# Kernel optimization log

Measured on AMD Instinct MI355X. Metric: run time of the kernel, lower is better.

Reference implementation:

```python
import jax, jax.numpy as jnp
import numpy as np

B, N, D, H, DEG = 2, 20000, 256, 8, 8
E = N * DEG
EPS = 1e-3  # keras LayerNormalization default epsilon


def layer_norm(x, gamma, beta):
    mu = jnp.mean(x, axis=-1, keepdims=True)
    var = jnp.mean(jnp.square(x - mu), axis=-1, keepdims=True)
    return (x - mu) * jax.lax.rsqrt(var + EPS) * gamma + beta


def setup_inputs() -> dict:
    key = jax.random.key(0)
    ks = jax.random.split(key, 8)
    x = jax.random.normal(ks[0], (B, N, D), dtype=jnp.float32)
    # edge list sorted by source node; every node has DEG out-edges so
    # segment_sum covers all N segments (matches tf.math.segment_sum semantics)
    src = jnp.repeat(jnp.arange(N, dtype=jnp.int64), DEG)
    dst = jax.random.randint(ks[1], (E,), 0, N, dtype=jnp.int64)
    edges = jnp.stack([src, dst], axis=1)  # [E, 2]
    scale = 0.05
    wq = jax.random.normal(ks[2], (D, D), dtype=jnp.float32) * scale
    wk = jax.random.normal(ks[3], (D, D), dtype=jnp.float32) * scale
    wv = jax.random.normal(ks[4], (D, D), dtype=jnp.float32) * scale
    wo = jax.random.normal(ks[5], (D, D), dtype=jnp.float32) * scale
    zeros = jnp.zeros((D,), dtype=jnp.float32)
    ones = jnp.ones((D,), dtype=jnp.float32)
    return {
        "x": x, "edges": edges,
        "wq": wq, "bq": zeros, "wk": wk, "bk": zeros,
        "wv": wv, "bv": zeros, "wo": wo, "bo": zeros,
        "gamma1": ones, "beta1": zeros, "gamma2": ones, "beta2": zeros,
    }


def reference(x, edges, wq, bq, wk, bk, wv, bv, wo, bo, gamma1, beta1, gamma2, beta2):
    b, n, d = x.shape
    h, dh = H, D // H
    xn = layer_norm(x, gamma1, beta1)                      # [B,N,D]
    # QKV projections, split heads, move node axis to front: [N,B,H,dh]
    def proj(w, bias):
        y = (xn @ w + bias).reshape(b, n, h, dh)
        return jnp.transpose(y, (1, 0, 2, 3))
    q, k, v = proj(wq, bq), proj(wk, bk), proj(wv, bv)
    src, dst = edges[:, 0], edges[:, 1]
    q_part = q[src]                                         # [E,B,H,dh]
    k_part = k[dst]
    v_part = v[dst]
    logits = jnp.sum(q_part * k_part, axis=-1, keepdims=True) / jnp.sqrt(
        jnp.asarray(dh, dtype=x.dtype))                     # [E,B,H,1]
    w = jnp.exp(logits)                                     # unnormalized softmax (as in source)
    num = jax.ops.segment_sum(v_part * w, src, num_segments=n)  # [N,B,H,dh]
    den = jax.ops.segment_sum(w, src, num_segments=n)           # [N,B,H,1]
    attn = num / den
    attn = jnp.transpose(attn, (1, 0, 2, 3)).reshape(b, n, d)   # [B,N,D]
    concat = xn + attn                                      # residual uses normed input (source reassigns `inputs`)
    out = layer_norm(concat, gamma2, beta2)
    out = jax.nn.relu(out @ wo + bo)
    return out + concat
```

## Files before the change

kernel.cpp:

```cpp
#include <hip/hip_runtime.h>
#include <hip/hip_bf16.h>

typedef __bf16 bf16x8 __attribute__((ext_vector_type(8)));
typedef float  f32x4  __attribute__((ext_vector_type(4)));

__device__ __forceinline__ float bf2f(unsigned short u) {
    union { unsigned int i; float f; } v; v.i = ((unsigned int)u) << 16; return v.f;
}
__device__ __forceinline__ unsigned short f2bf(float f) {
    union { float f; unsigned int i; } v; v.f = f;
    unsigned int x = v.i;
    unsigned int r = (x + 0x7FFFu + ((x >> 16) & 1u)) >> 16;
    return (unsigned short)r;
}

#define BF16_MAGIC 0x3F803F80u

template<bool BF16> __device__ __forceinline__ float ld1(const void* p, size_t i) {
    if constexpr (BF16) return bf2f(((const unsigned short*)p)[i]);
    else                return ((const float*)p)[i];
}
template<bool BF16> __device__ __forceinline__ float4 ld4v(const void* p, size_t i4) {
    if constexpr (BF16) {
        ushort4 u = ((const ushort4*)p)[i4];
        return make_float4(bf2f(u.x), bf2f(u.y), bf2f(u.z), bf2f(u.w));
    } else {
        return ((const float4*)p)[i4];
    }
}

#define NNODE 20000
#define ROWS  40000
#define DMODEL 256

template<bool BF16IN>
__global__ __launch_bounds__(256) void prep_kernel(
    const void* wq, const void* wk, const void* wv, const void* wo,
    const void* bq, const void* bk, const void* bv, const void* bo,
    const unsigned* __restrict__ mode,
    unsigned short* __restrict__ Wqkvt,
    unsigned short* __restrict__ Wot,
    float* __restrict__ biasq,
    float* __restrict__ biaso)
{
    if ((mode[0] == BF16_MAGIC) != BF16IN) return;
    int idx = blockIdx.x * 256 + threadIdx.x;
    if (idx < 768 * 256) {
        int n = idx >> 8, k = idx & 255;
        int sel = n >> 8, nl = n & 255;
        const void* w = (sel == 0) ? wq : (sel == 1) ? wk : wv;
        Wqkvt[idx] = f2bf(ld1<BF16IN>(w, k * 256 + nl));
    } else {
        int idx2 = idx - 768 * 256;
        int n = idx2 >> 8, k = idx2 & 255;
        Wot[idx2] = f2bf(ld1<BF16IN>(wo, k * 256 + n));
    }
    if (idx < 768) {
        const void* bb = (idx < 256) ? bq : (idx < 512) ? bk : bv;
        biasq[idx] = ld1<BF16IN>(bb, idx & 255);
    }
    if (idx >= 768 && idx < 1024) {
        biaso[idx - 768] = ld1<BF16IN>(bo, idx - 768);
    }
}

template<bool BF16IN>
__global__ __launch_bounds__(256) void ln1_kernel(
    const void* x, const void* g1, const void* b1,
    const unsigned* __restrict__ mode,
    unsigned short* __restrict__ xn)
{
    if ((mode[0] == BF16_MAGIC) != BF16IN) return;
    int wave = threadIdx.x >> 6, lane = threadIdx.x & 63;
    int m = blockIdx.x * 4 + wave;
    float4 f = ld4v<BF16IN>(x, (size_t)m * 64 + lane);
    float s  = f.x + f.y + f.z + f.w;
    float ss = f.x*f.x + f.y*f.y + f.z*f.z + f.w*f.w;
    #pragma unroll
    for (int mk = 1; mk < 64; mk <<= 1) { s += __shfl_xor(s, mk); ss += __shfl_xor(ss, mk); }
    float mu  = s * (1.f/256.f);
    float var = ss * (1.f/256.f) - mu*mu;
    float rs  = rsqrtf(var + 1e-3f);
    float4 g = ld4v<BF16IN>(g1, lane);
    float4 b = ld4v<BF16IN>(b1, lane);
    ushort4 o;
    o.x = f2bf((f.x - mu) * rs * g.x + b.x);
    o.y = f2bf((f.y - mu) * rs * g.y + b.y);
    o.z = f2bf((f.z - mu) * rs * g.z + b.z);
    o.w = f2bf((f.w - mu) * rs * g.w + b.w);
    *(ushort4*)(xn + (size_t)m * DMODEL + lane * 4) = o;
}

template<bool EPI, bool OUTBF16>
__global__ __launch_bounds__(256) void gemm_kernel(
    const unsigned short* __restrict__ A,
    const unsigned short* __restrict__ Bt,
    const float* __restrict__ bias,
    void* __restrict__ C,
    const unsigned short* __restrict__ resid,
    int Ncols,
    const unsigned* __restrict__ mode)
{
    if (EPI) { if ((mode[0] == BF16_MAGIC) != OUTBF16) return; }
    __shared__ unsigned short As[64][40];
    __shared__ unsigned short Bs[64][40];
    int tid  = threadIdx.x;
    int wave = tid >> 6, lane = tid & 63;
    int quad = lane >> 4, l16 = lane & 15;
    int m0 = blockIdx.x * 64;
    int n0 = blockIdx.y * 64;
    int sr = tid >> 2, sc = (tid & 3) * 8;

    const unsigned short* Ag = A  + (size_t)(m0 + sr) * 256 + sc;
    const unsigned short* Bg = Bt + (size_t)(n0 + sr) * 256 + sc;

    f32x4 acc[4] = {};

    for (int kt = 0; kt < 8; ++kt) {
        int4 av = *(const int4*)(Ag + kt * 32);
        int4 bv = *(const int4*)(Bg + kt * 32);
        __syncthreads();
        *(int4*)&As[sr][sc] = av;
        *(int4*)&Bs[sr][sc] = bv;
        __syncthreads();
        bf16x8 af = *(const bf16x8*)&As[wave * 16 + l16][quad * 8];
        #pragma unroll
        for (int ct = 0; ct < 4; ++ct) {
            bf16x8 bf = *(const bf16x8*)&Bs[ct * 16 + l16][quad * 8];
            acc[ct] = __builtin_amdgcn_mfma_f32_16x16x32_bf16(af, bf, acc[ct], 0, 0, 0);
        }
    }

    #pragma unroll
    for (int ct = 0; ct < 4; ++ct) {
        int col = n0 + ct * 16 + l16;
        float bb = bias[col];
        #pragma unroll
        for (int r = 0; r < 4; ++r) {
            int row = m0 + wave * 16 + quad * 4 + r;
            float v = acc[ct][r] + bb;
            if (EPI) {
                v = fmaxf(v, 0.f);
                v += bf2f(resid[(size_t)row * 256 + col]);
            }
            if (OUTBF16) ((unsigned short*)C)[(size_t)row * Ncols + col] = f2bf(v);
            else         ((float*)C)[(size_t)row * Ncols + col] = v;
        }
    }
}

template<bool BF16IN>
__global__ __launch_bounds__(256) void attn_kernel(
    const unsigned short* __restrict__ qkv,
    const int* __restrict__ edges,
    const unsigned short* __restrict__ xn,
    const void* g2, const void* b2,
    const unsigned* __restrict__ mode,
    unsigned short* __restrict__ concat,
    unsigned short* __restrict__ h2)
{
    if ((mode[0] == BF16_MAGIC) != BF16IN) return;
    int wave = threadIdx.x >> 6, lane = threadIdx.x & 63;
    int m = blockIdx.x * 4 + wave;
    int b = m / NNODE;
    int i = m - b * NNODE;
    int d0 = lane * 4;

    bool is64 = (edges[16] == 0);

    ushort4 qv = *(const ushort4*)(qkv + (size_t)m * 768 + d0);
    float q0 = bf2f(qv.x), q1 = bf2f(qv.y), q2 = bf2f(qv.z), q3 = bf2f(qv.w);

    int jv = 0;
    if (lane < 8) {
        int e = i * 8 + lane;
        jv = is64 ? edges[4 * e + 2] : edges[2 * e + 1];
    }

    float n0a = 0.f, n1a = 0.f, n2a = 0.f, n3a = 0.f, den = 0.f;
    const float scale = 0.17677669529663687f;
    #pragma unroll
    for (int e = 0; e < 8; ++e) {
        int j = __shfl(jv, e);
        size_t base = ((size_t)(b * NNODE + j)) * 768;
        ushort4 kv = *(const ushort4*)(qkv + base + 256 + d0);
        float dot = q0*bf2f(kv.x) + q1*bf2f(kv.y) + q2*bf2f(kv.z) + q3*bf2f(kv.w);
        dot += __shfl_xor(dot, 1);
        dot += __shfl_xor(dot, 2);
        dot += __shfl_xor(dot, 4);
        float w = __expf(dot * scale);
        ushort4 vv = *(const ushort4*)(qkv + base + 512 + d0);
        n0a += w * bf2f(vv.x); n1a += w * bf2f(vv.y);
        n2a += w * bf2f(vv.z); n3a += w * bf2f(vv.w);
        den += w;
    }
    float inv = 1.f / den;
    ushort4 xv = *(const ushort4*)(xn + (size_t)m * DMODEL + d0);
    float c0 = bf2f(xv.x) + n0a * inv;
    float c1 = bf2f(xv.y) + n1a * inv;
    float c2 = bf2f(xv.z) + n2a * inv;
    float c3 = bf2f(xv.w) + n3a * inv;

    float s  = c0 + c1 + c2 + c3;
    float ss = c0*c0 + c1*c1 + c2*c2 + c3*c3;
    #pragma unroll
    for (int mk = 1; mk < 64; mk <<= 1) { s += __shfl_xor(s, mk); ss += __shfl_xor(ss, mk); }
    float mu  = s * (1.f/256.f);
    float var = ss * (1.f/256.f) - mu*mu;
    float rs  = rsqrtf(var + 1e-3f);

    float4 g = ld4v<BF16IN>(g2, lane);
    float4 bb = ld4v<BF16IN>(b2, lane);
    ushort4 oc, oh;
    oc.x = f2bf(c0); oc.y = f2bf(c1); oc.z = f2bf(c2); oc.w = f2bf(c3);
    oh.x = f2bf((c0 - mu) * rs * g.x + bb.x);
    oh.y = f2bf((c1 - mu) * rs * g.y + bb.y);
    oh.z = f2bf((c2 - mu) * rs * g.z + bb.z);
    oh.w = f2bf((c3 - mu) * rs * g.w + bb.w);
    *(ushort4*)(concat + (size_t)m * DMODEL + d0) = oc;
    *(ushort4*)(h2     + (size_t)m * DMODEL + d0) = oh;
}

extern "C" void kernel_launch(void* const* d_in, const int* in_sizes, int n_in,
                              void* d_out, int out_size, void* d_ws, size_t ws_size,
                              hipStream_t stream)
{
    const void* x  = d_in[0];
    const int* edges = (const int*)d_in[1];
    const void* wq = d_in[2];  const void* bq = d_in[3];
    const void* wk = d_in[4];  const void* bk = d_in[5];
    const void* wv = d_in[6];  const void* bv = d_in[7];
    const void* wo = d_in[8];  const void* bo = d_in[9];
    const void* g1 = d_in[10]; const void* b1 = d_in[11];
    const void* g2 = d_in[12]; const void* b2 = d_in[13];
    const unsigned* mode = (const unsigned*)d_in[10];

    char* ws = (char*)d_ws;
    unsigned short* Wqkvt = (unsigned short*)(ws);
    unsigned short* Wot   = (unsigned short*)(ws + 393216);
    float* biasq          = (float*)(ws + 393216 + 131072);
    float* biaso          = (float*)(ws + 393216 + 131072 + 3072);
    size_t off = 393216 + 131072 + 4096;
    unsigned short* xn     = (unsigned short*)(ws + off); off += (size_t)ROWS * DMODEL * 2;
    unsigned short* qkv    = (unsigned short*)(ws + off); off += (size_t)ROWS * 768 * 2;
    unsigned short* concat = (unsigned short*)(ws + off); off += (size_t)ROWS * DMODEL * 2;
    unsigned short* h2     = (unsigned short*)(ws + off); off += (size_t)ROWS * DMODEL * 2;

    prep_kernel<true ><<<1024, 256, 0, stream>>>(wq, wk, wv, wo, bq, bk, bv, bo, mode, Wqkvt, Wot, biasq, biaso);
    prep_kernel<false><<<1024, 256, 0, stream>>>(wq, wk, wv, wo, bq, bk, bv, bo, mode, Wqkvt, Wot, biasq, biaso);
    ln1_kernel<true ><<<ROWS / 4, 256, 0, stream>>>(x, g1, b1, mode, xn);
    ln1_kernel<false><<<ROWS / 4, 256, 0, stream>>>(x, g1, b1, mode, xn);
    gemm_kernel<false, true><<<dim3(625, 12), 256, 0, stream>>>(xn, Wqkvt, biasq, qkv, nullptr, 768, mode);
    attn_kernel<true ><<<ROWS / 4, 256, 0, stream>>>(qkv, edges, xn, g2, b2, mode, concat, h2);
    attn_kernel<false><<<ROWS / 4, 256, 0, stream>>>(qkv, edges, xn, g2, b2, mode, concat, h2);
    gemm_kernel<true, true ><<<dim3(625, 4), 256, 0, stream>>>(h2, Wot, biaso, d_out, concat, 256, mode);
    gemm_kernel<true, false><<<dim3(625, 4), 256, 0, stream>>>(h2, Wot, biaso, d_out, concat, 256, mode);
}
```

Baseline: 249.8 us.

## Drop dtype-dispatch launches, enlarge GEMM tiles, widen per-lane vectors in LN and attention

Removes the runtime bf16/fp32 mode check and its duplicate kernel launches, hard-coding fp32 inputs and 32-bit edge indices. The GEMM moves from 64x64 to 128x128 tiles with 4x4 MFMA accumulators per wave, which raises operand reuse from LDS but leaves fewer blocks. The LayerNorm and attention kernels now give each lane 8 elements with 16-byte loads. Attention handles both batches of a node in one wave so the edge indices are shared. This drops the edges[16] check for 64-bit edges, so the code assumes int32 edge input.

```diff
diff --git a/kernel.cpp b/kernel.cpp
--- a/kernel.cpp
+++ b/kernel.cpp
@@ -1,5 +1,5 @@
 #include <hip/hip_runtime.h>
-#include <hip/hip_bf16.h>
+
 
 typedef __bf16 bf16x8 __attribute__((ext_vector_type(8)));
 typedef float  f32x4  __attribute__((ext_vector_type(4)));
@@ -14,226 +14,240 @@
     return (unsigned short)r;
 }
 
-#define BF16_MAGIC 0x3F803F80u
-
-template<bool BF16> __device__ __forceinline__ float ld1(const void* p, size_t i) {
-    if constexpr (BF16) return bf2f(((const unsigned short*)p)[i]);
-    else                return ((const float*)p)[i];
-}
-template<bool BF16> __device__ __forceinline__ float4 ld4v(const void* p, size_t i4) {
-    if constexpr (BF16) {
-        ushort4 u = ((const ushort4*)p)[i4];
-        return make_float4(bf2f(u.x), bf2f(u.y), bf2f(u.z), bf2f(u.w));
-    } else {
-        return ((const float4*)p)[i4];
-    }
-}
-
 #define NNODE 20000
 #define ROWS  40000
 #define DMODEL 256
 
-template<bool BF16IN>
 __global__ __launch_bounds__(256) void prep_kernel(
-    const void* wq, const void* wk, const void* wv, const void* wo,
-    const void* bq, const void* bk, const void* bv, const void* bo,
-    const unsigned* __restrict__ mode,
+    const float* __restrict__ wq, const float* __restrict__ wk,
+    const float* __restrict__ wv, const float* __restrict__ wo,
+    const float* __restrict__ bq, const float* __restrict__ bk,
+    const float* __restrict__ bv, const float* __restrict__ bo,
     unsigned short* __restrict__ Wqkvt,
     unsigned short* __restrict__ Wot,
     float* __restrict__ biasq,
     float* __restrict__ biaso)
 {
-    if ((mode[0] == BF16_MAGIC) != BF16IN) return;
     int idx = blockIdx.x * 256 + threadIdx.x;
     if (idx < 768 * 256) {
         int n = idx >> 8, k = idx & 255;
         int sel = n >> 8, nl = n & 255;
-        const void* w = (sel == 0) ? wq : (sel == 1) ? wk : wv;
-        Wqkvt[idx] = f2bf(ld1<BF16IN>(w, k * 256 + nl));
+        const float* w = (sel == 0) ? wq : (sel == 1) ? wk : wv;
+        Wqkvt[idx] = f2bf(w[k * 256 + nl]);
     } else {
         int idx2 = idx - 768 * 256;
         int n = idx2 >> 8, k = idx2 & 255;
-        Wot[idx2] = f2bf(ld1<BF16IN>(wo, k * 256 + n));
+        Wot[idx2] = f2bf(wo[k * 256 + n]);
     }
     if (idx < 768) {
-        const void* bb = (idx < 256) ? bq : (idx < 512) ? bk : bv;
-        biasq[idx] = ld1<BF16IN>(bb, idx & 255);
-    }
-    if (idx >= 768 && idx < 1024) {
-        biaso[idx - 768] = ld1<BF16IN>(bo, idx - 768);
-    }
-}
-
-template<bool BF16IN>
+        const float* bb = (idx < 256) ? bq : (idx < 512) ? bk : bv;
+        biasq[idx] = bb[idx & 255];
+    }
+    if (idx >= 768 && idx < 1024) biaso[idx - 768] = bo[idx - 768];
+}
+
 __global__ __launch_bounds__(256) void ln1_kernel(
-    const void* x, const void* g1, const void* b1,
-    const unsigned* __restrict__ mode,
+    const float* __restrict__ x,
+    const float* __restrict__ g1, const float* __restrict__ b1,
     unsigned short* __restrict__ xn)
 {
-    if ((mode[0] == BF16_MAGIC) != BF16IN) return;
     int wave = threadIdx.x >> 6, lane = threadIdx.x & 63;
-    int m = blockIdx.x * 4 + wave;
-    float4 f = ld4v<BF16IN>(x, (size_t)m * 64 + lane);
-    float s  = f.x + f.y + f.z + f.w;
-    float ss = f.x*f.x + f.y*f.y + f.z*f.z + f.w*f.w;
-    #pragma unroll
-    for (int mk = 1; mk < 64; mk <<= 1) { s += __shfl_xor(s, mk); ss += __shfl_xor(ss, mk); }
+    int sub = lane >> 5, hl = lane & 31;
+    int m = blockIdx.x * 8 + wave * 2 + sub;
+    const float* xp = x + (size_t)m * DMODEL + hl * 8;
+    float4 x0 = *(const float4*)xp;
+    float4 x1 = *(const float4*)(xp + 4);
+    float f[8] = {x0.x, x0.y, x0.z, x0.w, x1.x, x1.y, x1.z, x1.w};
+    float s = 0.f, ss = 0.f;
+    #pragma unroll
+    for (int t = 0; t < 8; ++t) { s += f[t]; ss += f[t]*f[t]; }
+    #pragma unroll
+    for (int mk = 1; mk < 32; mk <<= 1) { s += __shfl_xor(s, mk); ss += __shfl_xor(ss, mk); }
     float mu  = s * (1.f/256.f);
     float var = ss * (1.f/256.f) - mu*mu;
     float rs  = rsqrtf(var + 1e-3f);
-    float4 g = ld4v<BF16IN>(g1, lane);
-    float4 b = ld4v<BF16IN>(b1, lane);
-    ushort4 o;
-    o.x = f2bf((f.x - mu) * rs * g.x + b.x);
-    o.y = f2bf((f.y - mu) * rs * g.y + b.y);
-    o.z = f2bf((f.z - mu) * rs * g.z + b.z);
-    o.w = f2bf((f.w - mu) * rs * g.w + b.w);
-    *(ushort4*)(xn + (size_t)m * DMODEL + lane * 4) = o;
-}
-
-template<bool EPI, bool OUTBF16>
+    float4 g0 = *(const float4*)(g1 + hl * 8);
+    float4 g1v = *(const float4*)(g1 + hl * 8 + 4);
+    float4 b0 = *(const float4*)(b1 + hl * 8);
+    float4 b1v = *(const float4*)(b1 + hl * 8 + 4);
+    float gg[8] = {g0.x, g0.y, g0.z, g0.w, g1v.x, g1v.y, g1v.z, g1v.w};
+    float bb[8] = {b0.x, b0.y, b0.z, b0.w, b1v.x, b1v.y, b1v.z, b1v.w};
+    unsigned short o[8];
+    #pragma unroll
+    for (int t = 0; t < 8; ++t) o[t] = f2bf((f[t] - mu) * rs * gg[t] + bb[t]);
+    *(int4*)(xn + (size_t)m * DMODEL + hl * 8) = *(const int4*)o;
+}
+
+#define LDS_W 72
+template<bool EPI>
 __global__ __launch_bounds__(256) void gemm_kernel(
     const unsigned short* __restrict__ A,
     const unsigned short* __restrict__ Bt,
     const float* __restrict__ bias,
     void* __restrict__ C,
     const unsigned short* __restrict__ resid,
-    int Ncols,
-    const unsigned* __restrict__ mode)
-{
-    if (EPI) { if ((mode[0] == BF16_MAGIC) != OUTBF16) return; }
-    __shared__ unsigned short As[64][40];
-    __shared__ unsigned short Bs[64][40];
+    int M, int Ncols)
+{
+    __shared__ unsigned short As[128 * LDS_W];
+    __shared__ unsigned short Bs[128 * LDS_W];
     int tid  = threadIdx.x;
     int wave = tid >> 6, lane = tid & 63;
     int quad = lane >> 4, l16 = lane & 15;
-    int m0 = blockIdx.x * 64;
-    int n0 = blockIdx.y * 64;
-    int sr = tid >> 2, sc = (tid & 3) * 8;
-
-    const unsigned short* Ag = A  + (size_t)(m0 + sr) * 256 + sc;
-    const unsigned short* Bg = Bt + (size_t)(n0 + sr) * 256 + sc;
-
-    f32x4 acc[4] = {};
-
-    for (int kt = 0; kt < 8; ++kt) {
-        int4 av = *(const int4*)(Ag + kt * 32);
-        int4 bv = *(const int4*)(Bg + kt * 32);
+    int m0 = blockIdx.x * 128, n0 = blockIdx.y * 128;
+    int wm = (wave >> 1) * 64, wn = (wave & 1) * 64;
+
+    int srow = tid >> 1;
+    int sseg = (tid & 1) * 32;
+    int arow = m0 + srow; if (arow >= M) arow = M - 1;
+    const unsigned short* ArowP = A  + (size_t)arow * 256 + sseg;
+    const unsigned short* BrowP = Bt + (size_t)(n0 + srow) * 256 + sseg;
+    unsigned short* AsP = &As[srow * LDS_W + sseg];
+    unsigned short* BsP = &Bs[srow * LDS_W + sseg];
+
+    f32x4 acc[4][4] = {};
+
+    for (int kt = 0; kt < 4; ++kt) {
+        int4 a0[4], b0[4];
+        #pragma unroll
+        for (int i = 0; i < 4; ++i) a0[i] = *(const int4*)(ArowP + kt * 64 + i * 8);
+        #pragma unroll
+        for (int i = 0; i < 4; ++i) b0[i] = *(const int4*)(BrowP + kt * 64 + i * 8);
         __syncthreads();
-        *(int4*)&As[sr][sc] = av;
-        *(int4*)&Bs[sr][sc] = bv;
+        #pragma unroll
+        for (int i = 0; i < 4; ++i) *(int4*)(AsP + i * 8) = a0[i];
+        #pragma unroll
+        for (int i = 0; i < 4; ++i) *(int4*)(BsP + i * 8) = b0[i];
         __syncthreads();
-        bf16x8 af = *(const bf16x8*)&As[wave * 16 + l16][quad * 8];
-        #pragma unroll
-        for (int ct = 0; ct < 4; ++ct) {
-            bf16x8 bf = *(const bf16x8*)&Bs[ct * 16 + l16][quad * 8];
-            acc[ct] = __builtin_amdgcn_mfma_f32_16x16x32_bf16(af, bf, acc[ct], 0, 0, 0);
+        #pragma unroll
+        for (int ks = 0; ks < 2; ++ks) {
+            bf16x8 af[4], bfr[4];
+            #pragma unroll
+            for (int r = 0; r < 4; ++r) af[r]  = *(const bf16x8*)&As[(wm + r*16 + l16) * LDS_W + ks*32 + quad*8];
+            #pragma unroll
+            for (int c = 0; c < 4; ++c) bfr[c] = *(const bf16x8*)&Bs[(wn + c*16 + l16) * LDS_W + ks*32 + quad*8];
+            #pragma unroll
+            for (int r = 0; r < 4; ++r)
+                #pragma unroll
+                for (int c = 0; c < 4; ++c)
+                    acc[r][c] = __builtin_amdgcn_mfma_f32_16x16x32_bf16(af[r], bfr[c], acc[r][c], 0, 0, 0);
         }
     }
 
     #pragma unroll
-    for (int ct = 0; ct < 4; ++ct) {
-        int col = n0 + ct * 16 + l16;
+    for (int c = 0; c < 4; ++c) {
+        int col = n0 + wn + c * 16 + l16;
         float bb = bias[col];
         #pragma unroll
         for (int r = 0; r < 4; ++r) {
-            int row = m0 + wave * 16 + quad * 4 + r;
-            float v = acc[ct][r] + bb;
-            if (EPI) {
-                v = fmaxf(v, 0.f);
-                v += bf2f(resid[(size_t)row * 256 + col]);
+            int rowb = m0 + wm + r * 16 + quad * 4;
+            #pragma unroll
+            for (int rr = 0; rr < 4; ++rr) {
+                int row = rowb + rr;
+                if (row < M) {
+                    float v = acc[r][c][rr] + bb;
+                    if (EPI) {
+                        v = fmaxf(v, 0.f);
+                        v += bf2f(resid[(size_t)row * 256 + col]);
+                        ((float*)C)[(size_t)row * Ncols + col] = v;
+                    } else {
+                        ((unsigned short*)C)[(size_t)row * Ncols + col] = f2bf(v);
+                    }
+                }
             }
-            if (OUTBF16) ((unsigned short*)C)[(size_t)row * Ncols + col] = f2bf(v);
-            else         ((float*)C)[(size_t)row * Ncols + col] = v;
         }
     }
 }
 
-template<bool BF16IN>
 __global__ __launch_bounds__(256) void attn_kernel(
     const unsigned short* __restrict__ qkv,
     const int* __restrict__ edges,
     const unsigned short* __restrict__ xn,
-    const void* g2, const void* b2,
-    const unsigned* __restrict__ mode,
+    const float* __restrict__ g2, const float* __restrict__ b2,
     unsigned short* __restrict__ concat,
     unsigned short* __restrict__ h2)
 {
-    if ((mode[0] == BF16_MAGIC) != BF16IN) return;
     int wave = threadIdx.x >> 6, lane = threadIdx.x & 63;
-    int m = blockIdx.x * 4 + wave;
-    int b = m / NNODE;
-    int i = m - b * NNODE;
-    int d0 = lane * 4;
-
-    bool is64 = (edges[16] == 0);
-
-    ushort4 qv = *(const ushort4*)(qkv + (size_t)m * 768 + d0);
-    float q0 = bf2f(qv.x), q1 = bf2f(qv.y), q2 = bf2f(qv.z), q3 = bf2f(qv.w);
+    int i = blockIdx.x * 4 + wave;
+    int b = lane >> 5, hl = lane & 31;
+    size_t m = (size_t)b * NNODE + i;
+
+    int4 qi = *(const int4*)(qkv + m * 768 + hl * 8);
+    const unsigned short* qs = (const unsigned short*)&qi;
+    float qf[8];
+    #pragma unroll
+    for (int t = 0; t < 8; ++t) qf[t] = bf2f(qs[t]);
 
     int jv = 0;
-    if (lane < 8) {
-        int e = i * 8 + lane;
-        jv = is64 ? edges[4 * e + 2] : edges[2 * e + 1];
-    }
-
-    float n0a = 0.f, n1a = 0.f, n2a = 0.f, n3a = 0.f, den = 0.f;
+    if (lane < 8) jv = edges[2 * (i * 8 + lane) + 1];
+
+    float acc[8] = {};
+    float den = 0.f;
     const float scale = 0.17677669529663687f;
     #pragma unroll
     for (int e = 0; e < 8; ++e) {
         int j = __shfl(jv, e);
-        size_t base = ((size_t)(b * NNODE + j)) * 768;
-        ushort4 kv = *(const ushort4*)(qkv + base + 256 + d0);
-        float dot = q0*bf2f(kv.x) + q1*bf2f(kv.y) + q2*bf2f(kv.z) + q3*bf2f(kv.w);
+        const unsigned short* kp = qkv + ((size_t)b * NNODE + j) * 768 + 256 + hl * 8;
+        int4 ki = *(const int4*)kp;
+        int4 vi = *(const int4*)(kp + 256);
+        const unsigned short* ks = (const unsigned short*)&ki;
+        const unsigned short* vs = (const unsigned short*)&vi;
+        float dot = 0.f;
+        #pragma unroll
+        for (int t = 0; t < 8; ++t) dot += qf[t] * bf2f(ks[t]);
         dot += __shfl_xor(dot, 1);
         dot += __shfl_xor(dot, 2);
-        dot += __shfl_xor(dot, 4);
         float w = __expf(dot * scale);
-        ushort4 vv = *(const ushort4*)(qkv + base + 512 + d0);
-        n0a += w * bf2f(vv.x); n1a += w * bf2f(vv.y);
-        n2a += w * bf2f(vv.z); n3a += w * bf2f(vv.w);
+        #pragma unroll
+        for (int t = 0; t < 8; ++t) acc[t] += w * bf2f(vs[t]);
         den += w;
     }
     float inv = 1.f / den;
-    ushort4 xv = *(const ushort4*)(xn + (size_t)m * DMODEL + d0);
-    float c0 = bf2f(xv.x) + n0a * inv;
-    float c1 = bf2f(xv.y) + n1a * inv;
-    float c2 = bf2f(xv.z) + n2a * inv;
-    float c3 = bf2f(xv.w) + n3a * inv;
-
-    float s  = c0 + c1 + c2 + c3;
-    float ss = c0*c0 + c1*c1 + c2*c2 + c3*c3;
-    #pragma unroll
-    for (int mk = 1; mk < 64; mk <<= 1) { s += __shfl_xor(s, mk); ss += __shfl_xor(ss, mk); }
+
+    int4 xi = *(const int4*)(xn + m * DMODEL + hl * 8);
+    const unsigned short* xs = (const unsigned short*)&xi;
+    float c[8], s = 0.f, ss = 0.f;
+    #pragma unroll
+    for (int t = 0; t < 8; ++t) { c[t] = bf2f(xs[t]) + acc[t] * inv; s += c[t]; ss += c[t]*c[t]; }
+    #pragma unroll
+    for (int mk = 1; mk < 32; mk <<= 1) { s += __shfl_xor(s, mk); ss += __shfl_xor(ss, mk); }
     float mu  = s * (1.f/256.f);
     float var = ss * (1.f/256.f) - mu*mu;
     float rs  = rsqrtf(var + 1e-3f);
 
-    float4 g = ld4v<BF16IN>(g2, lane);
-    float4 bb = ld4v<BF16IN>(b2, lane);
-    ushort4 oc, oh;
-    oc.x = f2bf(c0); oc.y = f2bf(c1); oc.z = f2bf(c2); oc.w = f2bf(c3);
-    oh.x = f2bf((c0 - mu) * rs * g.x + bb.x);
-    oh.y = f2bf((c1 - mu) * rs * g.y + bb.y);
-    oh.z = f2bf((c2 - mu) * rs * g.z + bb.z);
-    oh.w = f2bf((c3 - mu) * rs * g.w + bb.w);
-    *(ushort4*)(concat + (size_t)m * DMODEL + d0) = oc;
-    *(ushort4*)(h2     + (size_t)m * DMODEL + d0) = oh;
+    float4 ga = *(const float4*)(g2 + hl * 8);
+    float4 gb = *(const float4*)(g2 + hl * 8 + 4);
+    float4 ba = *(const float4*)(b2 + hl * 8);
+    float4 bb = *(const float4*)(b2 + hl * 8 + 4);
+    float gg[8] = {ga.x, ga.y, ga.z, ga.w, gb.x, gb.y, gb.z, gb.w};
+    float bv[8] = {ba.x, ba.y, ba.z, ba.w, bb.x, bb.y, bb.z, bb.w};
+    unsigned short oc[8], oh[8];
+    #pragma unroll
+    for (int t = 0; t < 8; ++t) {
+        oc[t] = f2bf(c[t]);
+        oh[t] = f2bf((c[t] - mu) * rs * gg[t] + bv[t]);
+    }
+    *(int4*)(concat + m * DMODEL + hl * 8) = *(const int4*)oc;
+    *(int4*)(h2     + m * DMODEL + hl * 8) = *(const int4*)oh;
 }
 
 extern "C" void kernel_launch(void* const* d_in, const int* in_sizes, int n_in,
                               void* d_out, int out_size, void* d_ws, size_t ws_size,
                               hipStream_t stream)
 {
-    const void* x  = d_in[0];
+    const float* x   = (const float*)d_in[0];
     const int* edges = (const int*)d_in[1];
-    const void* wq = d_in[2];  const void* bq = d_in[3];
-    const void* wk = d_in[4];  const void* bk = d_in[5];
-    const void* wv = d_in[6];  const void* bv = d_in[7];
-    const void* wo = d_in[8];  const void* bo = d_in[9];
-    const void* g1 = d_in[10]; const void* b1 = d_in[11];
-    const void* g2 = d_in[12]; const void* b2 = d_in[13];
-    const unsigned* mode = (const unsigned*)d_in[10];
+    const float* wq = (const float*)d_in[2];
+    const float* bq = (const float*)d_in[3];
+    const float* wk = (const float*)d_in[4];
+    const float* bk = (const float*)d_in[5];
+    const float* wv = (const float*)d_in[6];
+    const float* bv = (const float*)d_in[7];
+    const float* wo = (const float*)d_in[8];
+    const float* bo = (const float*)d_in[9];
+    const float* g1 = (const float*)d_in[10];
+    const float* b1 = (const float*)d_in[11];
+    const float* g2 = (const float*)d_in[12];
+    const float* b2 = (const float*)d_in[13];
 
     char* ws = (char*)d_ws;
     unsigned short* Wqkvt = (unsigned short*)(ws);
@@ -246,13 +260,9 @@
     unsigned short* concat = (unsigned short*)(ws + off); off += (size_t)ROWS * DMODEL * 2;
     unsigned short* h2     = (unsigned short*)(ws + off); off += (size_t)ROWS * DMODEL * 2;
 
-    prep_kernel<true ><<<1024, 256, 0, stream>>>(wq, wk, wv, wo, bq, bk, bv, bo, mode, Wqkvt, Wot, biasq, biaso);
-    prep_kernel<false><<<1024, 256, 0, stream>>>(wq, wk, wv, wo, bq, bk, bv, bo, mode, Wqkvt, Wot, biasq, biaso);
-    ln1_kernel<true ><<<ROWS / 4, 256, 0, stream>>>(x, g1, b1, mode, xn);
-    ln1_kernel<false><<<ROWS / 4, 256, 0, stream>>>(x, g1, b1, mode, xn);
-    gemm_kernel<false, true><<<dim3(625, 12), 256, 0, stream>>>(xn, Wqkvt, biasq, qkv, nullptr, 768, mode);
-    attn_kernel<true ><<<ROWS / 4, 256, 0, stream>>>(qkv, edges, xn, g2, b2, mode, concat, h2);
-    attn_kernel<false><<<ROWS / 4, 256, 0, stream>>>(qkv, edges, xn, g2, b2, mode, concat, h2);
-    gemm_kernel<true, true ><<<dim3(625, 4), 256, 0, stream>>>(h2, Wot, biaso, d_out, concat, 256, mode);
-    gemm_kernel<true, false><<<dim3(625, 4), 256, 0, stream>>>(h2, Wot, biaso, d_out, concat, 256, mode);
-}
+    prep_kernel<<<1024, 256, 0, stream>>>(wq, wk, wv, wo, bq, bk, bv, bo, Wqkvt, Wot, biasq, biaso);
+    ln1_kernel<<<ROWS / 8, 256, 0, stream>>>(x, g1, b1, xn);
+    gemm_kernel<false><<<dim3(313, 6), 256, 0, stream>>>(xn, Wqkvt, biasq, qkv, nullptr, ROWS, 768);
+    attn_kernel<<<NNODE / 4, 256, 0, stream>>>(qkv, edges, xn, g2, b2, concat, h2);
+    gemm_kernel<true><<<dim3(313, 2), 256, 0, stream>>>(h2, Wot, biaso, d_out, concat, ROWS, 256);
+}
```

Result: slower. 354.9 us (+42.1%).
